# Performance work log

Measured on AMD Instinct MI355X. Metric: run time of the kernel, lower is better.

## Reference

```python
import jax, jax.numpy as jnp
import numpy as np

B, T, X, DC, DW, H = 64, 512, 8, 128, 128, 128
NEG = 1e20  # mask constant from the original '-1e20 trick'


def setup_inputs() -> dict:
    key = jax.random.key(0)
    ks = jax.random.split(key, 8)
    inp = jax.random.normal(ks[0], (B, T, DC), dtype=jnp.float32)
    skip_words = jax.random.normal(ks[1], (B, T, X, DW), dtype=jnp.float32)
    rng = np.random.default_rng(0)
    # skip edge source s at position t indexes history slot s+1, which must be <= t -> s <= t-1
    src = rng.integers(0, T, size=(B, T, X))
    src = np.minimum(src, np.maximum(np.arange(T) - 1, 0)[None, :, None]).astype(np.int32)
    cnt = np.minimum(rng.integers(0, X + 1, size=(B, T)), np.arange(T)[None, :]).astype(np.int32)
    s = 0.1
    return {
        'inp': inp,
        'skip_words': skip_words,
        'seq_len': jnp.full((B,), T, dtype=jnp.int32),
        'skip_sources': jnp.asarray(src),
        'skip_count': jnp.asarray(cnt),
        'w_ih_c': jax.random.normal(ks[2], (DC, 3 * H), dtype=jnp.float32) * s,
        'w_hh_c': jax.random.normal(ks[3], (H, 3 * H), dtype=jnp.float32) * s,
        'bias_c': jnp.zeros((3 * H,), dtype=jnp.float32),
        'a_ih': jax.random.normal(ks[4], (DC, H), dtype=jnp.float32) * s,
        'a_hh': jax.random.normal(ks[5], (H, H), dtype=jnp.float32) * s,
        'a_bias': jnp.zeros((H,), dtype=jnp.float32),
        'w_ih_w': jax.random.normal(ks[6], (DW, 3 * H), dtype=jnp.float32) * s,
        'w_hh_w': jax.random.normal(ks[7], (H, 3 * H), dtype=jnp.float32) * s,
        'bias_w': jnp.zeros((3 * H,), dtype=jnp.float32),
    }


def _forward(inp, skip_words, w_ih_c, w_hh_c, bias_c, a_ih, a_hh, a_bias,
             w_ih_w, w_hh_w, bias_w, skip_sources, skip_count):
    Bv, Tv, Xv, _ = skip_words.shape
    Hh = w_hh_c.shape[0]
    # Precompute all input projections (time-independent) outside the scan.
    wi_c_all = jnp.einsum('btd,dk->btk', inp, w_ih_c) + bias_c          # [B,T,3H]
    a_wi_all = jnp.einsum('btd,dh->bth', inp, a_ih) + a_bias            # [B,T,H]
    wi_w_all = jnp.einsum('btxd,dk->btxk', skip_words, w_ih_w) + bias_w  # [B,T,X,3H]
    iota = jnp.arange(Xv)

    def step(carry, xs):
        h_hist, c_hist = carry  # [B, T+1, H] states; slot t+1 written at step t
        t, wi_c, wi_w, a_wi, src, cnt = xs
        h0 = jnp.take(h_hist, t, axis=1)                                 # [B,H]
        idx = (src + 1)[:, :, None]                                      # skip_before_head=False
        c_x = jnp.take_along_axis(c_hist, idx, axis=1)                   # [B,X,H]
        h_x = jnp.take_along_axis(h_hist, idx, axis=1)                   # [B,X,H]
        # WordLSTMCell: c1 = sig(f)*c_x + sig(i)*tanh(g)
        gw = jnp.einsum('bxh,hk->bxk', h_x, w_hh_w) + wi_w               # [B,X,3H]
        f_w, i_w, g_w = jnp.split(gw, 3, axis=-1)
        c1_skip = jax.nn.sigmoid(f_w) * c_x + jax.nn.sigmoid(i_w) * jnp.tanh(g_w)
        # MultiInputLSTMCell: gated merge over {g} U skip cells
        gc = h0 @ w_hh_c + wi_c                                          # [B,3H]
        i_g, o_g, g_g = jnp.split(gc, 3, axis=-1)
        i_g = jax.nn.sigmoid(i_g)[:, None]                               # [B,1,H]
        o_g = jax.nn.sigmoid(o_g)                                        # [B,H]
        g_g = jnp.tanh(g_g)[:, None]                                     # [B,1,H]
        alpha = jax.nn.sigmoid(a_wi[:, None] + jnp.einsum('bxh,hk->bxk', c1_skip, a_hh))
        mask = (iota[None, :] >= cnt[:, None]).astype(alpha.dtype)[:, :, None] * NEG
        ealpha = jnp.exp(jnp.concatenate([i_g, alpha - mask], axis=1))   # [B,1+X,H]
        alpha_n = ealpha / ealpha.sum(axis=1, keepdims=True)
        merged = jnp.concatenate([g_g, c1_skip], axis=1)                 # [B,1+X,H]
        c1 = (merged * alpha_n).sum(axis=1)                              # [B,H]
        h1 = o_g * jnp.tanh(c1)
        h_hist = jax.lax.dynamic_update_slice(h_hist, h1[:, None], (0, t + 1, 0))
        c_hist = jax.lax.dynamic_update_slice(c_hist, c1[:, None], (0, t + 1, 0))
        return (h_hist, c_hist), (h1, c1)

    init = (jnp.zeros((Bv, Tv + 1, Hh), inp.dtype), jnp.zeros((Bv, Tv + 1, Hh), inp.dtype))
    xs = (jnp.arange(Tv), wi_c_all.swapaxes(0, 1), wi_w_all.swapaxes(0, 1),
          a_wi_all.swapaxes(0, 1), skip_sources.swapaxes(0, 1), skip_count.swapaxes(0, 1))
    _, (hs, cs) = jax.lax.scan(step, init, xs)
    return hs.swapaxes(0, 1), cs.swapaxes(0, 1)  # [B,T,H] each


def reference(inp, skip_words, w_ih_c, w_hh_c, bias_c, a_ih, a_hh, a_bias,
              w_ih_w, w_hh_w, bias_w, seq_len, skip_sources, skip_count):
    # seq_len only determines max_seq_len in the torch code; here T is static = inp.shape[1]
    return _forward(inp, skip_words, w_ih_c, w_hh_c, bias_c, a_ih, a_hh, a_bias,
                    w_ih_w, w_hh_w, bias_w, skip_sources, skip_count)
```

## Files before the change

kernel.cpp:

```cpp
#include <hip/hip_runtime.h>

typedef unsigned short u16;
typedef unsigned int u32;
typedef __attribute__((ext_vector_type(8))) short short8;
typedef __attribute__((ext_vector_type(4))) float f32x4;

constexpr int CB = 64, CT = 512, CX = 8, CH = 128;

__device__ __forceinline__ u16 f2b(float f) {
  u32 u = __float_as_uint(f);
  return (u16)((u + 0x7FFFu + ((u >> 16) & 1u)) >> 16);
}
__device__ __forceinline__ float sigf(float x) {
  return __fdividef(1.0f, 1.0f + __expf(-x));
}
__device__ __forceinline__ float tanhfast(float x) {
  return 1.0f - __fdividef(2.0f, __expf(2.0f * x) + 1.0f);
}
__device__ __forceinline__ f32x4 mfma16(short8 a, short8 b, f32x4 c) {
  return __builtin_amdgcn_mfma_f32_16x16x32_bf16(a, b, c, 0, 0, 0);
}


__global__ void prep_kernel(const float* __restrict__ w_ih_c, const float* __restrict__ w_hh_c,
                            const float* __restrict__ a_ih, const float* __restrict__ a_hh,
                            const float* __restrict__ w_ih_w, const float* __restrict__ w_hh_w,
                            u16* __restrict__ WgwT, u16* __restrict__ WahcT, u16* __restrict__ WcaT) {
  int gid = blockIdx.x * blockDim.x + threadIdx.x;
  if (gid < 98304) {
    int n = gid >> 8, k = gid & 255;
    float v = (k < 128) ? w_hh_w[k * 384 + n] : w_ih_w[(k - 128) * 384 + n];
    WgwT[gid] = f2b(v);
  } else if (gid < 163840) {
    int i = gid - 98304; int n = i >> 7, k = i & 127;
    float v = (n < 128) ? a_hh[k * 128 + n] : w_hh_c[k * 384 + (n - 128)];
    WahcT[i] = f2b(v);
  } else if (gid < 229376) {
    int i = gid - 163840; int n = i >> 7, k = i & 127;
    float v = (n < 384) ? w_ih_c[k * 384 + n] : a_ih[k * 128 + (n - 384)];
    WcaT[i] = f2b(v);
  }
}

__global__ __launch_bounds__(256) void proj_kernel(const float* __restrict__ inp,
    const u16* __restrict__ WcaT, const float* __restrict__ bias_c,
    const float* __restrict__ a_bias, float* __restrict__ wica) {
  const int m0 = blockIdx.x * 64;
  const int wv = threadIdx.x >> 6, ln = threadIdx.x & 63;
  const int l16 = ln & 15, qd = ln >> 4;
  const int arow = m0 + wv * 16 + l16;
  short8 af[4];
#pragma unroll
  for (int kt = 0; kt < 4; ++kt) {
    const float* p = inp + (size_t)arow * 128 + kt * 32 + qd * 8;
    float4 x0 = *(const float4*)p;
    float4 x1 = *(const float4*)(p + 4);
    short8 a;
    a[0] = (short)f2b(x0.x); a[1] = (short)f2b(x0.y); a[2] = (short)f2b(x0.z); a[3] = (short)f2b(x0.w);
    a[4] = (short)f2b(x1.x); a[5] = (short)f2b(x1.y); a[6] = (short)f2b(x1.z); a[7] = (short)f2b(x1.w);
    af[kt] = a;
  }
  for (int nt = 0; nt < 32; ++nt) {
    const int col = nt * 16 + l16;
    f32x4 acc = {0.f, 0.f, 0.f, 0.f};
#pragma unroll
    for (int kt = 0; kt < 4; ++kt) {
      short8 bf = *(const short8*)(WcaT + (size_t)col * 128 + kt * 32 + qd * 8);
      acc = mfma16(af[kt], bf, acc);
    }
    const float bias = (col < 384) ? bias_c[col] : a_bias[col - 384];
#pragma unroll
    for (int r = 0; r < 4; ++r) {
      const int orow = m0 + wv * 16 + qd * 4 + r;
      wica[(size_t)orow * 512 + col] = acc[r] + bias;
    }
  }
}

__global__ __launch_bounds__(512, 2) void scan_kernel(
    const float* __restrict__ skip_words,
    const int* __restrict__ srcp,
    const int* __restrict__ cntp,
    const float* __restrict__ bias_w,
    const u16* __restrict__ WgwT,
    const u16* __restrict__ WahcT,
    const float* __restrict__ wica,
    float* __restrict__ out)
{
  const int b = blockIdx.x;
  const int tid = threadIdx.x;
  const int wv = tid >> 6;
  const int ln = tid & 63;
  const int l16 = ln & 15;
  const int qd = ln >> 4;
  const int h = wv * 16 + l16;

  float* hs = out + (size_t)b * CT * CH;
  float* cs = out + (size_t)(CB + b) * CT * CH;
  const float* swb = skip_words + (size_t)b * CT * CX * CH;
  const int* srcb = srcp + b * CT * CX;
  const int* cntb = cntp + b * CT;
  const float* wicab = wica + (size_t)b * CT * 512;

  __shared__ __align__(16) u16 Asg[16 * 264];
  __shared__ __align__(16) u16 Psg[16 * 136];
  __shared__ __align__(16) float Csg[8 * 128];
  __shared__ __align__(16) u16 hprev[128];
  __shared__ __align__(16) float cprev[128];
  __shared__ float gca[512];

  for (int i = tid; i < 16 * 264; i += 512) Asg[i] = 0;
  for (int i = tid; i < 16 * 136; i += 512) Psg[i] = 0;
  if (tid < 128) { hprev[tid] = 0; cprev[tid] = 0.0f; }

  short8 wgwf[3][8];
#pragma unroll
  for (int g = 0; g < 3; ++g) {
    const int n = g * 128 + h;
#pragma unroll
    for (int kt = 0; kt < 8; ++kt)
      wgwf[g][kt] = *(const short8*)(WgwT + (size_t)n * 256 + kt * 32 + qd * 8);
  }
  short8 wacf[4][4];
#pragma unroll
  for (int j = 0; j < 4; ++j) {
    const int n = j * 128 + h;
#pragma unroll
    for (int kt = 0; kt < 4; ++kt)
      wacf[j][kt] = *(const short8*)(WahcT + (size_t)n * 128 + kt * 32 + qd * 8);
  }
  const float bw0 = bias_w[h], bw1 = bias_w[128 + h], bw2 = bias_w[256 + h];

  int src_c = srcb[wv];
  int cnt_c = cntb[0];
  int src_n = srcb[CX + wv];
  int cnt_n = cntb[1];
  float2 h2c, c2c, sw2c;
  h2c = *(const float2*)(hs + (size_t)src_c * CH + 2 * ln);
  c2c = *(const float2*)(cs + (size_t)src_c * CH + 2 * ln);
  sw2c = *(const float2*)(swb + (size_t)wv * CH + 2 * ln);
  float wicac = wicab[tid];
  float2 h2n = {0.f, 0.f}, c2n = {0.f, 0.f}, sw2n = {0.f, 0.f};
  float wican = 0.f;
  int src_n2 = 0, cnt_n2 = 0;
  __syncthreads();

  for (int t = 0; t < CT; ++t) {
    const bool fresh = (src_c == t - 1);
    if (fresh) {
      *(u32*)&Asg[wv * 264 + 2 * ln] = *(const u32*)&hprev[2 * ln];
      *(float2*)&Csg[wv * 128 + 2 * ln] = *(const float2*)&cprev[2 * ln];
    } else {
      *(u32*)&Asg[wv * 264 + 2 * ln] = (u32)f2b(h2c.x) | ((u32)f2b(h2c.y) << 16);
      *(float2*)&Csg[wv * 128 + 2 * ln] = c2c;
    }
    *(u32*)&Asg[wv * 264 + 128 + 2 * ln] = (u32)f2b(sw2c.x) | ((u32)f2b(sw2c.y) << 16);
    gca[tid] = wicac;
    if (wv == 7)
      *(u32*)&Psg[8 * 136 + 2 * ln] = *(const u32*)&hprev[2 * ln];
    __syncthreads();

    if (t + 1 < CT) {
      if (src_n != t) {
        h2n = *(const float2*)(hs + (size_t)src_n * CH + 2 * ln);
        c2n = *(const float2*)(cs + (size_t)src_n * CH + 2 * ln);
      }
      sw2n = *(const float2*)(swb + ((size_t)(t + 1) * CX + wv) * CH + 2 * ln);
      wican = wicab[(size_t)(t + 1) * 512 + tid];
      if (t + 2 < CT) { src_n2 = srcb[(t + 2) * CX + wv]; cnt_n2 = cntb[t + 2]; }
    }

    f32x4 d0 = {0.f, 0.f, 0.f, 0.f}, d1 = d0, d2 = d0;
#pragma unroll
    for (int kt = 0; kt < 8; ++kt) {
      short8 a = *(const short8*)&Asg[l16 * 264 + kt * 32 + qd * 8];
      d0 = mfma16(a, wgwf[0][kt], d0);
      d1 = mfma16(a, wgwf[1][kt], d1);
      d2 = mfma16(a, wgwf[2][kt], d2);
    }
    float c1s[4] = {0.f, 0.f, 0.f, 0.f};
    if (qd < 2) {
#pragma unroll
      for (int r = 0; r < 4; ++r) {
        const int row = qd * 4 + r;
        const float cx = Csg[row * 128 + h];
        const float fg = sigf(d0[r] + bw0);
        const float ig = sigf(d1[r] + bw1);
        const float gg = tanhfast(d2[r] + bw2);
        const float v = fg * cx + ig * gg;
        c1s[r] = v;
        Psg[row * 136 + h] = f2b(v);
      }
    }
    __syncthreads();

    f32x4 e0 = {0.f, 0.f, 0.f, 0.f}, e1 = e0, e2 = e0, e3 = e0;
#pragma unroll
    for (int kt = 0; kt < 4; ++kt) {
      short8 a = *(const short8*)&Psg[l16 * 136 + kt * 32 + qd * 8];
      e0 = mfma16(a, wacf[0][kt], e0);
      e1 = mfma16(a, wacf[1][kt], e1);
      e2 = mfma16(a, wacf[2][kt], e2);
      e3 = mfma16(a, wacf[3][kt], e3);
    }
    const float gi_d = __shfl(e1[0], 32 + l16, 64);
    const float go_d = __shfl(e2[0], 32 + l16, 64);
    const float gg_d = __shfl(e3[0], 32 + l16, 64);
    const float awi = gca[384 + h];
    const float i_g = sigf(gi_d + gca[h]);
    const float o_g = sigf(go_d + gca[128 + h]);
    const float g_g = tanhfast(gg_d + gca[256 + h]);
    float pe = 0.0f, pec = 0.0f;
#pragma unroll
    for (int r = 0; r < 4; ++r) {
      const int row = qd * 4 + r;
      if (row < cnt_c) {
        const float al = sigf(e0[r] + awi);
        const float e = __expf(al);
        pe += e;
        pec += e * c1s[r];
      }
    }
    pe += __shfl_xor(pe, 16, 64);  pec += __shfl_xor(pec, 16, 64);
    pe += __shfl_xor(pe, 32, 64);  pec += __shfl_xor(pec, 32, 64);
    const float ei = __expf(i_g);
    const float c1 = __fdividef(ei * g_g + pec, ei + pe);
    const float h1 = o_g * tanhfast(c1);

    if (qd == 0) {
      hs[(size_t)t * CH + h] = h1;
      cs[(size_t)t * CH + h] = c1;
      hprev[h] = f2b(h1);
      cprev[h] = c1;
    }
    __syncthreads();

    h2c = h2n; c2c = c2n; sw2c = sw2n; wicac = wican;
    src_c = src_n; cnt_c = cnt_n; src_n = src_n2; cnt_n = cnt_n2;
  }
}

extern "C" void kernel_launch(void* const* d_in, const int* in_sizes, int n_in,
                              void* d_out, int out_size, void* d_ws, size_t ws_size,
                              hipStream_t stream) {
  (void)in_sizes; (void)n_in; (void)out_size; (void)ws_size;
  const float* inp    = (const float*)d_in[0];
  const float* skw    = (const float*)d_in[1];
  const int*   ssrc   = (const int*)d_in[3];
  const int*   scnt   = (const int*)d_in[4];
  const float* w_ih_c = (const float*)d_in[5];
  const float* w_hh_c = (const float*)d_in[6];
  const float* bias_c = (const float*)d_in[7];
  const float* a_ih   = (const float*)d_in[8];
  const float* a_hh   = (const float*)d_in[9];
  const float* a_bias = (const float*)d_in[10];
  const float* w_ih_w = (const float*)d_in[11];
  const float* w_hh_w = (const float*)d_in[12];
  const float* bias_w = (const float*)d_in[13];

  char* ws = (char*)d_ws;
  u16*   WgwT  = (u16*)(ws);
  u16*   WahcT = (u16*)(ws + 196608);
  u16*   WcaT  = (u16*)(ws + 327680);
  float* wica  = (float*)(ws + 458752);
  float* out   = (float*)d_out;

  prep_kernel<<<224, 1024, 0, stream>>>(w_ih_c, w_hh_c, a_ih, a_hh, w_ih_w, w_hh_w,
                                        WgwT, WahcT, WcaT);
  proj_kernel<<<512, 256, 0, stream>>>(inp, WcaT, bias_c, a_bias, wica);
  scan_kernel<<<64, 512, 0, stream>>>(skw, ssrc, scnt, bias_w, WgwT, WahcT, wica, out);
}
```

Measured before the change: 1.446 ms.

## Pack two batch sequences per block and restructure scan step synchronization

Each scan block now processes two batch elements, filling all 16 MFMA rows (8 skip edges per sequence) instead of 8 real rows plus padding. The step drops from three barriers to two. Next-step skip state is written directly into the operand tiles, and freshly produced h/c values are forwarded into rows that reference the previous step. The LDS tiles use XOR swizzling instead of padding, and the h history tile is double-buffered. This halves the grid to 32 blocks and lowers the occupancy hint, so fewer CUs are used and each block's serial step does more work.

Measured after the change: 2.168 ms. +50.0%, slower.

```diff
diff --git a/kernel.cpp b/kernel.cpp
--- a/kernel.cpp
+++ b/kernel.cpp
@@ -11,6 +11,9 @@
   u32 u = __float_as_uint(f);
   return (u16)((u + 0x7FFFu + ((u >> 16) & 1u)) >> 16);
 }
+__device__ __forceinline__ u32 pack2bf(float2 v) {
+  return (u32)f2b(v.x) | ((u32)f2b(v.y) << 16);
+}
 __device__ __forceinline__ float sigf(float x) {
   return __fdividef(1.0f, 1.0f + __expf(-x));
 }
@@ -19,6 +22,12 @@
 }
 __device__ __forceinline__ f32x4 mfma16(short8 a, short8 b, f32x4 c) {
   return __builtin_amdgcn_mfma_f32_16x16x32_bf16(a, b, c, 0, 0, 0);
+}
+__device__ __forceinline__ int aswz(int row, int k) {
+  return row * 256 + ((k & 0xC0) | ((((k >> 3) ^ row) & 7) << 3) | (k & 7));
+}
+__device__ __forceinline__ int pswz(int row, int k) {
+  return row * 128 + ((k & 0x40) | ((((k >> 3) ^ (row & 7)) & 7) << 3) | (k & 7));
 }
 
 
@@ -77,7 +86,7 @@
   }
 }
 
-__global__ __launch_bounds__(512, 2) void scan_kernel(
+__global__ __launch_bounds__(512, 1) void scan_kernel(
     const float* __restrict__ skip_words,
     const int* __restrict__ srcp,
     const int* __restrict__ cntp,
@@ -87,31 +96,31 @@
     const float* __restrict__ wica,
     float* __restrict__ out)
 {
-  const int b = blockIdx.x;
+  const int b0 = 2 * blockIdx.x;
   const int tid = threadIdx.x;
   const int wv = tid >> 6;
   const int ln = tid & 63;
   const int l16 = ln & 15;
   const int qd = ln >> 4;
   const int h = wv * 16 + l16;
-
-  float* hs = out + (size_t)b * CT * CH;
-  float* cs = out + (size_t)(CB + b) * CT * CH;
-  const float* swb = skip_words + (size_t)b * CT * CX * CH;
-  const int* srcb = srcp + b * CT * CX;
-  const int* cntb = cntp + b * CT;
-  const float* wicab = wica + (size_t)b * CT * 512;
-
-  __shared__ __align__(16) u16 Asg[16 * 264];
-  __shared__ __align__(16) u16 Psg[16 * 136];
-  __shared__ __align__(16) float Csg[8 * 128];
-  __shared__ __align__(16) u16 hprev[128];
-  __shared__ __align__(16) float cprev[128];
-  __shared__ float gca[512];
-
-  for (int i = tid; i < 16 * 264; i += 512) Asg[i] = 0;
-  for (int i = tid; i < 16 * 136; i += 512) Psg[i] = 0;
-  if (tid < 128) { hprev[tid] = 0; cprev[tid] = 0.0f; }
+  const int beta = qd >> 1;
+  const int qh = qd & 1;
+
+  float* hs0 = out + (size_t)b0 * CT * CH;           float* hs1 = hs0 + CT * CH;
+  float* cs0 = out + (size_t)(CB + b0) * CT * CH;    float* cs1 = cs0 + CT * CH;
+  const float* sw0 = skip_words + (size_t)b0 * CT * CX * CH;  const float* sw1 = sw0 + (size_t)CT * CX * CH;
+  const int* sr0 = srcp + b0 * CT * CX;  const int* sr1 = sr0 + CT * CX;
+  const int* cn0 = cntp + b0 * CT;       const int* cn1 = cn0 + CT;
+  const float* wicme = wica + (size_t)(b0 + beta) * CT * 512;
+  float* hsme = beta ? hs1 : hs0;
+  float* csme = beta ? cs1 : cs0;
+
+  __shared__ __align__(16) u16 Asg[16 * 256];
+  __shared__ __align__(16) u16 Psg[16 * 128];
+  __shared__ __align__(16) u16 Gsg[2][16 * 128];
+  __shared__ __align__(16) float Csg[16 * 132];
+
+  for (int i = tid; i < 2 * 16 * 128 / 2; i += 512) ((u32*)Gsg)[i] = 0;
 
   short8 wgwf[3][8];
 #pragma unroll
@@ -121,122 +130,165 @@
     for (int kt = 0; kt < 8; ++kt)
       wgwf[g][kt] = *(const short8*)(WgwT + (size_t)n * 256 + kt * 32 + qd * 8);
   }
-  short8 wacf[4][4];
-#pragma unroll
-  for (int j = 0; j < 4; ++j) {
-    const int n = j * 128 + h;
+  short8 waca[4];
+#pragma unroll
+  for (int kt = 0; kt < 4; ++kt)
+    waca[kt] = *(const short8*)(WahcT + (size_t)h * 128 + kt * 32 + qd * 8);
+  short8 wacc[3][4];
+#pragma unroll
+  for (int g = 0; g < 3; ++g) {
+    const int n = 128 + g * 128 + h;
 #pragma unroll
     for (int kt = 0; kt < 4; ++kt)
-      wacf[j][kt] = *(const short8*)(WahcT + (size_t)n * 128 + kt * 32 + qd * 8);
+      wacc[g][kt] = *(const short8*)(WahcT + (size_t)n * 128 + kt * 32 + qd * 8);
   }
   const float bw0 = bias_w[h], bw1 = bias_w[128 + h], bw2 = bias_w[256 + h];
 
-  int src_c = srcb[wv];
-  int cnt_c = cntb[0];
-  int src_n = srcb[CX + wv];
-  int cnt_n = cntb[1];
-  float2 h2c, c2c, sw2c;
-  h2c = *(const float2*)(hs + (size_t)src_c * CH + 2 * ln);
-  c2c = *(const float2*)(cs + (size_t)src_c * CH + 2 * ln);
-  sw2c = *(const float2*)(swb + (size_t)wv * CH + 2 * ln);
-  float wicac = wicab[tid];
-  float2 h2n = {0.f, 0.f}, c2n = {0.f, 0.f}, sw2n = {0.f, 0.f};
-  float wican = 0.f;
-  int src_n2 = 0, cnt_n2 = 0;
+  int srcF0, srcF1;
+  {
+    int s00 = sr0[wv], s01 = sr1[wv];
+    float2 hA = *(const float2*)(hs0 + (size_t)s00 * CH + 2 * ln);
+    float2 cA = *(const float2*)(cs0 + (size_t)s00 * CH + 2 * ln);
+    float2 hB = *(const float2*)(hs1 + (size_t)s01 * CH + 2 * ln);
+    float2 cB = *(const float2*)(cs1 + (size_t)s01 * CH + 2 * ln);
+    float2 wA = *(const float2*)(sw0 + (size_t)wv * CH + 2 * ln);
+    float2 wB = *(const float2*)(sw1 + (size_t)wv * CH + 2 * ln);
+    *(u32*)&Asg[aswz(wv, 2 * ln)] = pack2bf(hA);
+    *(u32*)&Asg[aswz(wv, 128 + 2 * ln)] = pack2bf(wA);
+    *(float2*)&Csg[wv * 132 + 2 * ln] = cA;
+    *(u32*)&Asg[aswz(8 + wv, 2 * ln)] = pack2bf(hB);
+    *(u32*)&Asg[aswz(8 + wv, 128 + 2 * ln)] = pack2bf(wB);
+    *(float2*)&Csg[(8 + wv) * 132 + 2 * ln] = cB;
+    srcF0 = sr0[CX + wv];
+    srcF1 = sr1[CX + wv];
+  }
   __syncthreads();
 
   for (int t = 0; t < CT; ++t) {
-    const bool fresh = (src_c == t - 1);
-    if (fresh) {
-      *(u32*)&Asg[wv * 264 + 2 * ln] = *(const u32*)&hprev[2 * ln];
-      *(float2*)&Csg[wv * 128 + 2 * ln] = *(const float2*)&cprev[2 * ln];
-    } else {
-      *(u32*)&Asg[wv * 264 + 2 * ln] = (u32)f2b(h2c.x) | ((u32)f2b(h2c.y) << 16);
-      *(float2*)&Csg[wv * 128 + 2 * ln] = c2c;
-    }
-    *(u32*)&Asg[wv * 264 + 128 + 2 * ln] = (u32)f2b(sw2c.x) | ((u32)f2b(sw2c.y) << 16);
-    gca[tid] = wicac;
-    if (wv == 7)
-      *(u32*)&Psg[8 * 136 + 2 * ln] = *(const u32*)&hprev[2 * ln];
-    __syncthreads();
-
-    if (t + 1 < CT) {
-      if (src_n != t) {
-        h2n = *(const float2*)(hs + (size_t)src_n * CH + 2 * ln);
-        c2n = *(const float2*)(cs + (size_t)src_n * CH + 2 * ln);
-      }
-      sw2n = *(const float2*)(swb + ((size_t)(t + 1) * CX + wv) * CH + 2 * ln);
-      wican = wicab[(size_t)(t + 1) * 512 + tid];
-      if (t + 2 < CT) { src_n2 = srcb[(t + 2) * CX + wv]; cnt_n2 = cntb[t + 2]; }
+    const int cntv0 = cn0[t], cntv1 = cn1[t];
+    const float wi0 = wicme[(size_t)t * 512 + h];
+    const float wi1 = wicme[(size_t)t * 512 + 128 + h];
+    const float wi2 = wicme[(size_t)t * 512 + 256 + h];
+    const float wi3 = wicme[(size_t)t * 512 + 384 + h];
+    const bool st = (t + 1 < CT);
+    const bool fr0 = (srcF0 == t), fr1 = (srcF1 == t);
+    float2 hA = {0.f, 0.f}, cA = {0.f, 0.f}, hB = {0.f, 0.f}, cB = {0.f, 0.f};
+    float2 wA = {0.f, 0.f}, wB = {0.f, 0.f};
+    int fm0 = 0, fm1 = 0, srcFn0 = 0, srcFn1 = 0;
+    if (st) {
+      if (!fr0) {
+        hA = *(const float2*)(hs0 + (size_t)srcF0 * CH + 2 * ln);
+        cA = *(const float2*)(cs0 + (size_t)srcF0 * CH + 2 * ln);
+      }
+      if (!fr1) {
+        hB = *(const float2*)(hs1 + (size_t)srcF1 * CH + 2 * ln);
+        cB = *(const float2*)(cs1 + (size_t)srcF1 * CH + 2 * ln);
+      }
+      wA = *(const float2*)(sw0 + ((size_t)(t + 1) * CX + wv) * CH + 2 * ln);
+      wB = *(const float2*)(sw1 + ((size_t)(t + 1) * CX + wv) * CH + 2 * ln);
+      int4 a0 = *(const int4*)(sr0 + (t + 1) * CX);
+      int4 a1 = *(const int4*)(sr0 + (t + 1) * CX + 4);
+      int4 b0v = *(const int4*)(sr1 + (t + 1) * CX);
+      int4 b1v = *(const int4*)(sr1 + (t + 1) * CX + 4);
+      fm0 = (a0.x == t) | ((a0.y == t) << 1) | ((a0.z == t) << 2) | ((a0.w == t) << 3) |
+            ((a1.x == t) << 4) | ((a1.y == t) << 5) | ((a1.z == t) << 6) | ((a1.w == t) << 7);
+      fm1 = (b0v.x == t) | ((b0v.y == t) << 1) | ((b0v.z == t) << 2) | ((b0v.w == t) << 3) |
+            ((b1v.x == t) << 4) | ((b1v.y == t) << 5) | ((b1v.z == t) << 6) | ((b1v.w == t) << 7);
+      if (t + 2 < CT) { srcFn0 = sr0[(t + 2) * CX + wv]; srcFn1 = sr1[(t + 2) * CX + wv]; }
     }
 
     f32x4 d0 = {0.f, 0.f, 0.f, 0.f}, d1 = d0, d2 = d0;
 #pragma unroll
     for (int kt = 0; kt < 8; ++kt) {
-      short8 a = *(const short8*)&Asg[l16 * 264 + kt * 32 + qd * 8];
+      short8 a = *(const short8*)&Asg[aswz(l16, kt * 32 + qd * 8)];
       d0 = mfma16(a, wgwf[0][kt], d0);
       d1 = mfma16(a, wgwf[1][kt], d1);
       d2 = mfma16(a, wgwf[2][kt], d2);
     }
-    float c1s[4] = {0.f, 0.f, 0.f, 0.f};
-    if (qd < 2) {
-#pragma unroll
-      for (int r = 0; r < 4; ++r) {
-        const int row = qd * 4 + r;
-        const float cx = Csg[row * 128 + h];
-        const float fg = sigf(d0[r] + bw0);
-        const float ig = sigf(d1[r] + bw1);
-        const float gg = tanhfast(d2[r] + bw2);
-        const float v = fg * cx + ig * gg;
-        c1s[r] = v;
-        Psg[row * 136 + h] = f2b(v);
-      }
-    }
-    __syncthreads();
-
-    f32x4 e0 = {0.f, 0.f, 0.f, 0.f}, e1 = e0, e2 = e0, e3 = e0;
-#pragma unroll
-    for (int kt = 0; kt < 4; ++kt) {
-      short8 a = *(const short8*)&Psg[l16 * 136 + kt * 32 + qd * 8];
-      e0 = mfma16(a, wacf[0][kt], e0);
-      e1 = mfma16(a, wacf[1][kt], e1);
-      e2 = mfma16(a, wacf[2][kt], e2);
-      e3 = mfma16(a, wacf[3][kt], e3);
-    }
-    const float gi_d = __shfl(e1[0], 32 + l16, 64);
-    const float go_d = __shfl(e2[0], 32 + l16, 64);
-    const float gg_d = __shfl(e3[0], 32 + l16, 64);
-    const float awi = gca[384 + h];
-    const float i_g = sigf(gi_d + gca[h]);
-    const float o_g = sigf(go_d + gca[128 + h]);
-    const float g_g = tanhfast(gg_d + gca[256 + h]);
-    float pe = 0.0f, pec = 0.0f;
+    float c1s[4];
 #pragma unroll
     for (int r = 0; r < 4; ++r) {
       const int row = qd * 4 + r;
-      if (row < cnt_c) {
-        const float al = sigf(e0[r] + awi);
+      const float cx = Csg[row * 132 + h];
+      const float fg = sigf(d0[r] + bw0);
+      const float ig = sigf(d1[r] + bw1);
+      const float gg = tanhfast(d2[r] + bw2);
+      const float v = fg * cx + ig * gg;
+      c1s[r] = v;
+      Psg[pswz(row, h)] = f2b(v);
+    }
+    asm volatile("s_waitcnt lgkmcnt(0)\n\ts_barrier" ::: "memory");
+
+    f32x4 e0 = {0.f, 0.f, 0.f, 0.f}, e1 = e0, e2 = e0, e3 = e0;
+    const u16* Gr = Gsg[t & 1];
+#pragma unroll
+    for (int kt = 0; kt < 4; ++kt) {
+      short8 p = *(const short8*)&Psg[pswz(l16, kt * 32 + qd * 8)];
+      e0 = mfma16(p, waca[kt], e0);
+      short8 g = *(const short8*)&Gr[pswz(l16, kt * 32 + qd * 8)];
+      e1 = mfma16(g, wacc[0][kt], e1);
+      e2 = mfma16(g, wacc[1][kt], e2);
+      e3 = mfma16(g, wacc[2][kt], e3);
+    }
+    if (st) {
+      if (!fr0) {
+        *(u32*)&Asg[aswz(wv, 2 * ln)] = pack2bf(hA);
+        *(float2*)&Csg[wv * 132 + 2 * ln] = cA;
+      }
+      *(u32*)&Asg[aswz(wv, 128 + 2 * ln)] = pack2bf(wA);
+      if (!fr1) {
+        *(u32*)&Asg[aswz(8 + wv, 2 * ln)] = pack2bf(hB);
+        *(float2*)&Csg[(8 + wv) * 132 + 2 * ln] = cB;
+      }
+      *(u32*)&Asg[aswz(8 + wv, 128 + 2 * ln)] = pack2bf(wB);
+    }
+
+    const float ga0 = __shfl(e1[0], l16, 64), ga1 = __shfl(e1[1], l16, 64);
+    const float gb0 = __shfl(e2[0], l16, 64), gb1 = __shfl(e2[1], l16, 64);
+    const float gc0 = __shfl(e3[0], l16, 64), gc1 = __shfl(e3[1], l16, 64);
+    const float gi_d = beta ? ga1 : ga0;
+    const float go_d = beta ? gb1 : gb0;
+    const float gg_d = beta ? gc1 : gc0;
+    const float i_g = sigf(gi_d + wi0);
+    const float o_g = sigf(go_d + wi1);
+    const float g_g = tanhfast(gg_d + wi2);
+    const int cnt = beta ? cntv1 : cntv0;
+    float pe = 0.f, pec = 0.f;
+#pragma unroll
+    for (int r = 0; r < 4; ++r) {
+      const int rowb = qh * 4 + r;
+      if (rowb < cnt) {
+        const float al = sigf(e0[r] + wi3);
         const float e = __expf(al);
         pe += e;
         pec += e * c1s[r];
       }
     }
-    pe += __shfl_xor(pe, 16, 64);  pec += __shfl_xor(pec, 16, 64);
-    pe += __shfl_xor(pe, 32, 64);  pec += __shfl_xor(pec, 32, 64);
+    pe += __shfl_xor(pe, 16, 64);
+    pec += __shfl_xor(pec, 16, 64);
     const float ei = __expf(i_g);
     const float c1 = __fdividef(ei * g_g + pec, ei + pe);
     const float h1 = o_g * tanhfast(c1);
 
-    if (qd == 0) {
-      hs[(size_t)t * CH + h] = h1;
-      cs[(size_t)t * CH + h] = c1;
-      hprev[h] = f2b(h1);
-      cprev[h] = c1;
+    u16* Gw = Gsg[(t + 1) & 1];
+    if (!qh) {
+      hsme[(size_t)t * CH + h] = h1;
+      csme[(size_t)t * CH + h] = c1;
+      Gw[pswz(beta, h)] = f2b(h1);
+      const int fm = beta ? fm1 : fm0;
+      if (fm) {
+        const u16 hb = f2b(h1);
+#pragma unroll
+        for (int s = 0; s < 8; ++s)
+          if ((fm >> s) & 1) {
+            Asg[aswz(beta * 8 + s, h)] = hb;
+            Csg[(beta * 8 + s) * 132 + h] = c1;
+          }
+      }
     }
     __syncthreads();
-
-    h2c = h2n; c2c = c2n; sw2c = sw2n; wicac = wican;
-    src_c = src_n; cnt_c = cnt_n; src_n = src_n2; cnt_n = cnt_n2;
+    srcF0 = srcFn0;
+    srcF1 = srcFn1;
   }
 }
 
@@ -268,5 +320,5 @@
   prep_kernel<<<224, 1024, 0, stream>>>(w_ih_c, w_hh_c, a_ih, a_hh, w_ih_w, w_hh_w,
                                         WgwT, WahcT, WcaT);
   proj_kernel<<<512, 256, 0, stream>>>(inp, WcaT, bias_c, a_bias, wica);
-  scan_kernel<<<64, 512, 0, stream>>>(skw, ssrc, scnt, bias_w, WgwT, WahcT, wica, out);
-}
+  scan_kernel<<<32, 512, 0, stream>>>(skw, ssrc, scnt, bias_w, WgwT, WahcT, wica, out);
+}
```
